# Kernel tuning notes

Hardware: AMD Instinct MI355X
Metric: run time of the kernel (lower is better)

Reference implementation:

```python
import jax, jax.numpy as jnp
import numpy as np

HEADS = 8
DIM_HEAD = 64


def setup_inputs() -> dict:
    key = jax.random.key(0)
    ks = jax.random.split(key, 5)
    B, N, C, coor = 2, 2048, 256, 3
    dim_inner = HEADS * DIM_HEAD  # 512
    # weight scale 1/16 ~ 1/sqrt(256) keeps softmax logits in a sane range
    w_scale = 1.0 / 16.0
    return {
        "x": jax.random.normal(ks[0], (B, N, C, coor), dtype=jnp.float32),
        "Wq": jax.random.normal(ks[1], (dim_inner, C), dtype=jnp.float32) * w_scale,
        "Wk": jax.random.normal(ks[2], (dim_inner, C), dtype=jnp.float32) * w_scale,
        "Wv": jax.random.normal(ks[3], (dim_inner, C), dtype=jnp.float32) * w_scale,
        "Wo": jax.random.normal(ks[4], (C, dim_inner), dtype=jnp.float32) * w_scale,
    }


def _split_heads(t, B, N, coor):
    # b n (h d) c -> b h n (d c)
    t = t.reshape(B, N, HEADS, DIM_HEAD, coor)
    t = t.transpose(0, 2, 1, 3, 4)
    return t.reshape(B, HEADS, N, DIM_HEAD * coor)


def reference(x, Wq, Wk, Wv, Wo):
    B, N, C, coor = x.shape
    # VNLinear: einsum('... i c, o i -> ... o c')
    q = jnp.einsum('bnic,oi->bnoc', x, Wq)
    k = jnp.einsum('bnic,oi->bnoc', x, Wk)
    v = jnp.einsum('bnic,oi->bnoc', x, Wv)
    q = _split_heads(q, B, N, coor)  # (B, H, N, d*c)
    k = _split_heads(k, B, N, coor)
    v = _split_heads(v, B, N, coor)
    scale = (DIM_HEAD * coor) ** -0.5
    sim = jnp.einsum('bhie,bhje->bhij', q, k) * scale  # (B, H, N, N)
    attn = jax.nn.softmax(sim, axis=-1)
    out = jnp.einsum('bhij,bhje->bhie', attn, v)  # (B, H, N, d*c)
    # b h n (d c) -> b n (h d) c
    out = out.reshape(B, HEADS, N, DIM_HEAD, coor).transpose(0, 2, 1, 3, 4)
    out = out.reshape(B, N, HEADS * DIM_HEAD, coor)
    # to_out VNLinear
    return jnp.einsum('bnic,oi->bnoc', out, Wo)  # (B, N, C, 3)
```

## Files before the change

kernel.cpp:

```cpp
#include <hip/hip_runtime.h>

#define HEADS 8
#define DH 64
#define CO 3
#define E 192
#define NSEQ 2048
#define BATCH 2
#define CIN 256
#define DINNER 512
#define NTOK 4096
#define BHTOT 16

typedef __attribute__((ext_vector_type(8))) short bf16x8;
typedef __attribute__((ext_vector_type(4))) short bf16x4;
typedef __attribute__((ext_vector_type(4))) float f32x4;
typedef __attribute__((ext_vector_type(4))) float float4v;

static __device__ inline short f2bf(float f) {
  union { float f; unsigned u; } v; v.f = f;
  unsigned r = (v.u + 0x7FFFu + ((v.u >> 16) & 1u)) >> 16;
  return (short)r;
}

static __device__ inline float bf2f(short s) {
  union { unsigned u; float f; } a;
  a.u = ((unsigned)(unsigned short)s) << 16;
  return a.f;
}

static __device__ inline void load_lds16(const short* g, short* l) {
  __builtin_amdgcn_global_load_lds(
      (const __attribute__((address_space(1))) void*)g,
      (__attribute__((address_space(3))) void*)l, 16, 0, 0);
}


__global__ __launch_bounds__(256) void prep(const float* __restrict__ x,
                                            const float* __restrict__ Wq,
                                            const float* __restrict__ Wk,
                                            const float* __restrict__ Wv,
                                            const float* __restrict__ Wo,
                                            short* __restrict__ xcp,
                                            short* __restrict__ wqkvp,
                                            short* __restrict__ wop) {
  int tid = threadIdx.x;
  if (blockIdx.x < 256) {
    __shared__ short st[12288];
    int mt = blockIdx.x;
    const float* xb = x + (size_t)mt * 12288;
#pragma unroll
    for (int r = 0; r < 12; r++) {
      int idx4 = r * 256 + tid;
      float4v v = *(const float4v*)(xb + idx4 * 4);
#pragma unroll
      for (int e = 0; e < 4; e++) {
        int fp = idx4 * 4 + e;
        int ti = fp / 3, c = fp - ti * 3;
        int tl = ti >> 8, i = ti & 255;
        int ks = i >> 5, qd = (i >> 3) & 3, j = i & 7;
        st[c * 4096 + ks * 512 + (qd * 16 + tl) * 8 + j] = f2bf(v[e]);
      }
    }
    __syncthreads();
    short* dst = xcp;
#pragma unroll
    for (int rep = 0; rep < 6; rep++) {
      int g = rep * 256 + tid;
      int c = g >> 9, rem = g & 511;
      *(bf16x8*)(dst + ((size_t)(c * 256 + mt) * 8) * 512 + rem * 8) =
          *(const bf16x8*)&st[c * 4096 + rem * 8];
    }
    return;
  }
  int idx = (blockIdx.x - 256) * 256 + tid;
  const float qscale = 0.07216878364870323f * 1.4426950408889634f;
  if (idx < 1536 * 256) {
    int o = idx >> 8, i = idx & 255;
    float v;
    if (o < 512) v = Wq[idx] * qscale;
    else if (o < 1024) v = Wk[idx - 512 * 256];
    else v = Wv[idx - 1024 * 256];
    int nt = o >> 4, ln = o & 15, ks = i >> 5, qd = (i >> 3) & 3, j = i & 7;
    wqkvp[((size_t)(nt * 8 + ks)) * 512 + (qd * 16 + ln) * 8 + j] = f2bf(v);
  } else {
    int j0 = idx - 1536 * 256;
    if (j0 < 256 * 512) {
      int o2 = j0 >> 9, i = j0 & 511;
      int nt = o2 >> 4, ln = o2 & 15, ks = i >> 5, qd = (i >> 3) & 3, j = i & 7;
      wop[((size_t)(nt * 16 + ks)) * 512 + (qd * 16 + ln) * 8 + j] = f2bf(Wo[j0]);
    }
  }
}

__global__ __launch_bounds__(256, 4) void qkv_gemm(const short* __restrict__ xcp,
                                                   const short* __restrict__ wqkvp,
                                                   short* __restrict__ qp,
                                                   short* __restrict__ kp,
                                                   short* __restrict__ vp) {
  __shared__ __align__(16) short pool[9216];
  int c = blockIdx.z, ntb = blockIdx.x, mtb = blockIdx.y;
  int tid = threadIdx.x, wave = tid >> 6, lane = tid & 63;
  int ln = lane & 15, quad = lane >> 4;
  int wm = wave >> 1, wn = wave & 1;

  const short* gA = xcp + ((size_t)(c * 256 + mtb * 8) * 8) * 512;

  f32x4 acc[4][2] = {};
#pragma unroll
  for (int i = 0; i < 2; i++) {
    int q = tid + 256 * i, mf = q >> 6, l = q & 63;
    load_lds16(gA + (size_t)(mf * 8) * 512 + l * 8, pool + q * 8);
  }
  for (int ks = 0; ks < 8; ks++) {
    int b = ks & 1;
    __syncthreads();
    if (ks < 7) {
#pragma unroll
      for (int i = 0; i < 2; i++) {
        int q = tid + 256 * i, mf = q >> 6, l = q & 63;
        load_lds16(gA + (size_t)(mf * 8 + ks + 1) * 512 + l * 8,
                   pool + (b ^ 1) * 4096 + q * 8);
      }
    }
    const short* As = pool + b * 4096;
    bf16x8 af[4], bfr[2];
#pragma unroll
    for (int j = 0; j < 2; j++)
      bfr[j] = *(const bf16x8*)(wqkvp +
          (size_t)((ntb * 4 + wn * 2 + j) * 8 + ks) * 512 + lane * 8);
#pragma unroll
    for (int i = 0; i < 4; i++) af[i] = *(const bf16x8*)&As[(wm * 4 + i) * 512 + lane * 8];
#pragma unroll
    for (int i = 0; i < 4; i++)
#pragma unroll
      for (int j = 0; j < 2; j++)
        acc[i][j] = __builtin_amdgcn_mfma_f32_16x16x32_bf16(af[i], bfr[j], acc[i][j], 0, 0, 0);
  }

  int mat = ntb >> 3;
  int h = ntb & 7;
  int b0 = mtb >> 4;
  int bhx = b0 * 8 + h;
  if (mat < 2) {
    __syncthreads();
    short* tp = pool;
#pragma unroll
    for (int i = 0; i < 4; i++)
#pragma unroll
      for (int j = 0; j < 2; j++)
#pragma unroll
        for (int jj = 0; jj < 4; jj++)
          tp[(wm * 64 + i * 16 + quad * 4 + jj) * 72 + wn * 32 + j * 16 + ln] =
              f2bf(acc[i][j][jj]);
    __syncthreads();
    short* dst = (mat == 0) ? qp : kp;
#pragma unroll
    for (int rep = 0; rep < 4; rep++) {
      int gi = rep * 256 + tid;
      int l2 = gi & 15, qd = (gi >> 4) & 3, nf2 = (gi >> 6) & 3,
          esp = (gi >> 8) & 1, kt2 = (gi >> 9) & 1;
      int tl = kt2 * 64 + nf2 * 16 + l2;
      bf16x8 val = *(const bf16x8*)&tp[tl * 72 + esp * 32 + qd * 8];
      int kt = (mtb * 2 + kt2) & 31;
      int es = c * 2 + esp;
      size_t off = (((size_t)((bhx * 32 + kt) * 24) + es * 4 + nf2) * 64 +
                    (size_t)(qd * 16 + l2)) * 8;
      *(bf16x8*)(dst + off) = val;
    }
  } else {
    int q2 = quad ^ (((quad ^ (quad >> 1)) & 1) * 3);
#pragma unroll
    for (int i = 0; i < 4; i++) {
      int kt = (mtb * 2 + wm) & 31;
      int ks2 = (i >> 1) & 1;
      int qd2 = (i * 2 + (q2 >> 1)) & 3;
#pragma unroll
      for (int j = 0; j < 2; j++) {
        int ef = c * 4 + wn * 2 + j;
        size_t off = ((size_t)((bhx * 32 + kt) * 24 + ks2 * 12 + ef)) * 512 +
                     (qd2 * 16 + ln) * 8 + (q2 & 1) * 4;
        bf16x4 val = { f2bf(acc[i][j][0]), f2bf(acc[i][j][1]),
                       f2bf(acc[i][j][2]), f2bf(acc[i][j][3]) };
        *(bf16x4*)(vp + off) = val;
      }
    }
  }
}

__global__ __launch_bounds__(256, 2) void attn(const short* __restrict__ qp,
                                               const short* __restrict__ kp,
                                               const short* __restrict__ vp,
                                               short* __restrict__ opart,
                                               float* __restrict__ lpart) {
  __shared__ __align__(16) short pool[36864];
  int pair = blockIdx.x, qt = blockIdx.y;
  int bh = pair & 15, kh = pair >> 4;
  int tid = threadIdx.x, wave = tid >> 6, lane = tid & 63;
  int ln = lane & 15, quad = lane >> 4;

  bf16x8 qf[2][6];
#pragma unroll
  for (int rg = 0; rg < 2; rg++) {
    int fi = wave * 2 + rg;
    const short* qb = qp +
        ((size_t)(bh * 32 + qt * 2 + (fi >> 2)) * 24 + (fi & 3)) * 512 + lane * 8;
#pragma unroll
    for (int es = 0; es < 6; es++) qf[rg][es] = *(const bf16x8*)(qb + es * 2048);
  }

  float l_r[2] = {0.f, 0.f};
  f32x4 acc[2][12] = {};
  bf16x8 pa[2] = {};
  const short* gKb = kp + (size_t)(bh * 32 + kh * 16) * 12288;
  const short* gVb = vp + (size_t)(bh * 32 + kh * 16) * 12288;

  auto stage_k = [&](int k32) {
    const short* g64 = gKb + (size_t)(k32 >> 1) * 12288;
    int half = k32 & 1;
    short* Kd = pool + (k32 % 3) * 6144;
#pragma unroll
    for (int i = 0; i < 3; i++) {
      int q = i * 256 + tid;
      int f = q >> 6, l = q & 63;
      int es = f >> 1, nfl = f & 1;
      load_lds16(g64 + (size_t)(es * 4 + half * 2 + nfl) * 512 + l * 8, Kd + q * 8);
    }
  };
  auto stage_v = [&](int k32) {
    const short* g64 = gVb + (size_t)(k32 >> 1) * 12288;
    int half = k32 & 1;
    short* Vd = pool + 18432 + (k32 % 3) * 6144;
#pragma unroll
    for (int i = 0; i < 3; i++) {
      int q = i * 256 + tid;
      int f = q >> 6, l = q & 63;
      load_lds16(g64 + (size_t)(half * 12 + f) * 512 + l * 8, Vd + q * 8);
    }
  };

  stage_k(0);
  stage_k(1);
  stage_v(0);
  for (int kt = 0; kt < 32; kt++) {
    asm volatile("s_waitcnt vmcnt(6)" ::: "memory");
    __builtin_amdgcn_s_barrier();
    asm volatile("" ::: "memory");
    if (kt < 30) stage_k(kt + 2);
    if (kt < 31) stage_v(kt + 1);
    const short* Kl = pool + (kt % 3) * 6144;
    const short* Vl = pool + 18432 + ((kt + 2) % 3) * 6144;

    __builtin_amdgcn_s_setprio(1);
    f32x4 s[2][2] = {};
#pragma unroll
    for (int es = 0; es < 6; es++) {
#pragma unroll
      for (int nfl = 0; nfl < 2; nfl++) {
        bf16x8 kf = *(const bf16x8*)&Kl[(es * 2 + nfl) * 512 + lane * 8];
        s[0][nfl] = __builtin_amdgcn_mfma_f32_16x16x32_bf16(kf, qf[0][es], s[0][nfl], 0, 0, 0);
        s[1][nfl] = __builtin_amdgcn_mfma_f32_16x16x32_bf16(kf, qf[1][es], s[1][nfl], 0, 0, 0);
      }
    }
    if (kt > 0) {
#pragma unroll
      for (int ef = 0; ef < 12; ef++) {
        bf16x8 v0 = *(const bf16x8*)&Vl[ef * 512 + lane * 8];
        acc[0][ef] = __builtin_amdgcn_mfma_f32_16x16x32_bf16(pa[0], v0, acc[0][ef], 0, 0, 0);
        acc[1][ef] = __builtin_amdgcn_mfma_f32_16x16x32_bf16(pa[1], v0, acc[1][ef], 0, 0, 0);
      }
    }
    __builtin_amdgcn_s_setprio(0);

#pragma unroll
    for (int rg = 0; rg < 2; rg++) {
      float p0[4], p1[4];
#pragma unroll
      for (int jj = 0; jj < 4; jj++) {
        float e0 = __builtin_amdgcn_exp2f(s[rg][0][jj]);
        float e1 = __builtin_amdgcn_exp2f(s[rg][1][jj]);
        p0[jj] = e0; p1[jj] = e1;
        l_r[rg] += e0;
        l_r[rg] += e1;
      }
      unsigned a0, a1, b0, b1;
      asm("v_cvt_pk_bf16_f32 %0, %1, %2" : "=v"(a0) : "v"(p0[0]), "v"(p0[1]));
      asm("v_cvt_pk_bf16_f32 %0, %1, %2" : "=v"(a1) : "v"(p0[2]), "v"(p0[3]));
      asm("v_cvt_pk_bf16_f32 %0, %1, %2" : "=v"(b0) : "v"(p1[0]), "v"(p1[1]));
      asm("v_cvt_pk_bf16_f32 %0, %1, %2" : "=v"(b1) : "v"(p1[2]), "v"(p1[3]));
      auto r0 = __builtin_amdgcn_permlane32_swap(a0, b0, false, false);
      auto r1 = __builtin_amdgcn_permlane32_swap(a1, b1, false, false);
      union { unsigned u[4]; bf16x8 v; } pk;
      pk.u[0] = r0[0]; pk.u[1] = r1[0]; pk.u[2] = r0[1]; pk.u[3] = r1[1];
      pa[rg] = pk.v;
    }
  }

  __syncthreads();
  {
    const short* Vl = pool + 18432 + 6144;
#pragma unroll
    for (int ef = 0; ef < 12; ef++) {
      bf16x8 v0 = *(const bf16x8*)&Vl[ef * 512 + lane * 8];
      acc[0][ef] = __builtin_amdgcn_mfma_f32_16x16x32_bf16(pa[0], v0, acc[0][ef], 0, 0, 0);
      acc[1][ef] = __builtin_amdgcn_mfma_f32_16x16x32_bf16(pa[1], v0, acc[1][ef], 0, 0, 0);
    }
  }

#pragma unroll
  for (int rg = 0; rg < 2; rg++) {
    l_r[rg] += __shfl_xor(l_r[rg], 16, 64);
    l_r[rg] += __shfl_xor(l_r[rg], 32, 64);
  }

  __syncthreads();
  short* tp = pool;
#pragma unroll
  for (int rg = 0; rg < 2; rg++)
#pragma unroll
    for (int jj = 0; jj < 4; jj++) {
      int row = (wave * 2 + rg) * 16 + quad * 4 + jj;
#pragma unroll
      for (int ef = 0; ef < 12; ef++)
        tp[row * 200 + ef * 16 + ln] = f2bf(acc[rg][ef][jj]);
    }
  __syncthreads();
  const size_t obase = ((size_t)(kh * 16 + bh) * 2048 + qt * 128) * 192;
#pragma unroll
  for (int rep = 0; rep < 12; rep++) {
    int gi = rep * 256 + tid;
    int row = gi / 24, c8 = gi - row * 24;
    *(bf16x8*)(opart + obase + (size_t)row * 192 + c8 * 8) =
        *(const bf16x8*)&tp[row * 200 + c8 * 8];
  }
  int lb = (kh * 16 + bh) * 2048 + qt * 128;
  if (quad == 0) {
#pragma unroll
    for (int rg = 0; rg < 2; rg++)
      lpart[lb + (wave * 2 + rg) * 16 + ln] = l_r[rg];
  }
}

__global__ __launch_bounds__(256) void out_gemm(const short* __restrict__ opart,
                                                const float* __restrict__ lpart,
                                                const short* __restrict__ wop,
                                                float* __restrict__ out) {
  __shared__ __align__(16) float pool_f[12352];
  short* Al = (short*)pool_f;
  int mtb = blockIdx.x;
  int tid = threadIdx.x, wave = tid >> 6, lane = tid & 63;
  int ln = lane & 15, quad = lane >> 4;
  const size_t HSTR = (size_t)16 * 2048 * 192;

#pragma unroll
  for (int rep = 0; rep < 12; rep++) {
    int g = rep * 256 + tid;
    int c = g >> 10, inner = g & 1023;
    int d8 = inner & 7, h = (inner >> 3) & 7, row16 = inner >> 6;
    int t = mtb * 16 + row16, b = t >> 11, n = t & 2047;
    int bh = b * 8 + h;
    size_t src = ((size_t)bh * 2048 + n) * 192 + c * 64 + d8 * 8;
    bf16x8 o1 = *(const bf16x8*)(opart + src);
    bf16x8 o2 = *(const bf16x8*)(opart + HSTR + src);
    float l = lpart[bh * 2048 + n] + lpart[32768 + bh * 2048 + n];
    float inv = 1.f / l;
    bf16x8 r;
#pragma unroll
    for (int j = 0; j < 8; j++) r[j] = f2bf((bf2f(o1[j]) + bf2f(o2[j])) * inv);
    int ks = h * 2 + (d8 >> 2), qd = d8 & 3;
    *(bf16x8*)&Al[c * 8192 + ks * 512 + (qd * 16 + row16) * 8] = r;
  }
  __syncthreads();

  f32x4 acc[3][4] = {};
  for (int ks = 0; ks < 16; ks++) {
    bf16x8 af[3];
#pragma unroll
    for (int c = 0; c < 3; c++) af[c] = *(const bf16x8*)&Al[c * 8192 + ks * 512 + lane * 8];
#pragma unroll
    for (int jf = 0; jf < 4; jf++) {
      int nt = wave * 4 + jf;
      bf16x8 bfr = *(const bf16x8*)(wop + (size_t)(nt * 16 + ks) * 512 + lane * 8);
#pragma unroll
      for (int c = 0; c < 3; c++)
        acc[c][jf] = __builtin_amdgcn_mfma_f32_16x16x32_bf16(af[c], bfr, acc[c][jf], 0, 0, 0);
    }
  }
  __syncthreads();
#pragma unroll
  for (int c = 0; c < 3; c++)
#pragma unroll
    for (int jf = 0; jf < 4; jf++) {
      int o2 = (wave * 4 + jf) * 16 + ln;
#pragma unroll
      for (int jj = 0; jj < 4; jj++)
        pool_f[(quad * 4 + jj) * 772 + o2 * 3 + c] = acc[c][jf][jj];
    }
  __syncthreads();
  float* ob = out + (size_t)mtb * 12288;
#pragma unroll
  for (int rep = 0; rep < 12; rep++) {
    int idx = rep * 256 + tid;
    int row = idx / 192, col4 = idx - row * 192;
    *(float4v*)(ob + row * 768 + col4 * 4) =
        *(const float4v*)(pool_f + row * 772 + col4 * 4);
  }
}

extern "C" void kernel_launch(void* const* d_in, const int* in_sizes, int n_in,
                              void* d_out, int out_size, void* d_ws, size_t ws_size,
                              hipStream_t stream) {
  const float* x  = (const float*)d_in[0];
  const float* Wq = (const float*)d_in[1];
  const float* Wk = (const float*)d_in[2];
  const float* Wv = (const float*)d_in[3];
  const float* Wo = (const float*)d_in[4];
  float* out = (float*)d_out;

  short* ws    = (short*)d_ws;
  short* xcp   = ws;
  short* wqkvp = xcp + 3 * NTOK * CIN;
  short* wop   = wqkvp + 1536 * 256;
  short* qp    = wop + 256 * 512;
  short* kp    = qp + (size_t)BHTOT * NSEQ * E;
  short* vp    = kp + (size_t)BHTOT * NSEQ * E;
  short* opart = vp + (size_t)BHTOT * NSEQ * E;
  float* lpart = (float*)xcp;

  prep<<<2304, 256, 0, stream>>>(x, Wq, Wk, Wv, Wo, xcp, wqkvp, wop);
  qkv_gemm<<<dim3(24, 32, 3), 256, 0, stream>>>(xcp, wqkvp, qp, kp, vp);
  attn<<<dim3(32, 16), 256, 0, stream>>>(qp, kp, vp, opart, lpart);
  out_gemm<<<256, 256, 0, stream>>>(opart, lpart, wop, out);
}
```

Baseline: 155.8 us.

## Load V fragments directly from global into registers, drop LDS V staging

V tiles are now read by each wave straight from global memory into registers instead of being staged through LDS. The PV MFMA now runs in the same iteration as the QK product, replacing the one-iteration-delayed software pipeline. This shrinks LDS use and removes the V LDS reads. In exchange it adds 12 vector registers per lane, and each of the four waves loads the same V data from global/L2 separately. K staging keeps a triple buffer, plus a dummy fourth slot for the tail prefetches.

```diff
diff --git a/kernel.cpp b/kernel.cpp
--- a/kernel.cpp
+++ b/kernel.cpp
@@ -192,7 +192,7 @@
                                                const short* __restrict__ vp,
                                                short* __restrict__ opart,
                                                float* __restrict__ lpart) {
-  __shared__ __align__(16) short pool[36864];
+  __shared__ __align__(16) short pool[25600];
   int pair = blockIdx.x, qt = blockIdx.y;
   int bh = pair & 15, kh = pair >> 4;
   int tid = threadIdx.x, wave = tid >> 6, lane = tid & 63;
@@ -210,14 +210,13 @@
 
   float l_r[2] = {0.f, 0.f};
   f32x4 acc[2][12] = {};
-  bf16x8 pa[2] = {};
   const short* gKb = kp + (size_t)(bh * 32 + kh * 16) * 12288;
   const short* gVb = vp + (size_t)(bh * 32 + kh * 16) * 12288;
 
-  auto stage_k = [&](int k32) {
+  auto stage_k = [&](int k32, int slot) {
     const short* g64 = gKb + (size_t)(k32 >> 1) * 12288;
     int half = k32 & 1;
-    short* Kd = pool + (k32 % 3) * 6144;
+    short* Kd = pool + slot * 6144;
 #pragma unroll
     for (int i = 0; i < 3; i++) {
       int q = i * 256 + tid;
@@ -226,30 +225,24 @@
       load_lds16(g64 + (size_t)(es * 4 + half * 2 + nfl) * 512 + l * 8, Kd + q * 8);
     }
   };
-  auto stage_v = [&](int k32) {
-    const short* g64 = gVb + (size_t)(k32 >> 1) * 12288;
-    int half = k32 & 1;
-    short* Vd = pool + 18432 + (k32 % 3) * 6144;
-#pragma unroll
-    for (int i = 0; i < 3; i++) {
-      int q = i * 256 + tid;
-      int f = q >> 6, l = q & 63;
-      load_lds16(g64 + (size_t)(half * 12 + f) * 512 + l * 8, Vd + q * 8);
-    }
-  };
-
-  stage_k(0);
-  stage_k(1);
-  stage_v(0);
+
+  stage_k(0, 0);
+  stage_k(1, 1);
   for (int kt = 0; kt < 32; kt++) {
-    asm volatile("s_waitcnt vmcnt(6)" ::: "memory");
+    asm volatile("s_waitcnt vmcnt(3)" ::: "memory");
     __builtin_amdgcn_s_barrier();
     asm volatile("" ::: "memory");
-    if (kt < 30) stage_k(kt + 2);
-    if (kt < 31) stage_v(kt + 1);
+
+    const short* gV64 = gVb + (size_t)(kt >> 1) * 12288 + (size_t)(kt & 1) * 6144;
+    bf16x8 vr[12];
+#pragma unroll
+    for (int ef = 0; ef < 12; ef++)
+      vr[ef] = *(const bf16x8*)(gV64 + ef * 512 + lane * 8);
+    asm volatile("" ::: "memory");
+    stage_k((kt + 2) & 31, (kt < 30) ? ((kt + 2) % 3) : 3);
+    asm volatile("" ::: "memory");
+
     const short* Kl = pool + (kt % 3) * 6144;
-    const short* Vl = pool + 18432 + ((kt + 2) % 3) * 6144;
-
     __builtin_amdgcn_s_setprio(1);
     f32x4 s[2][2] = {};
 #pragma unroll
@@ -261,16 +254,9 @@
         s[1][nfl] = __builtin_amdgcn_mfma_f32_16x16x32_bf16(kf, qf[1][es], s[1][nfl], 0, 0, 0);
       }
     }
-    if (kt > 0) {
-#pragma unroll
-      for (int ef = 0; ef < 12; ef++) {
-        bf16x8 v0 = *(const bf16x8*)&Vl[ef * 512 + lane * 8];
-        acc[0][ef] = __builtin_amdgcn_mfma_f32_16x16x32_bf16(pa[0], v0, acc[0][ef], 0, 0, 0);
-        acc[1][ef] = __builtin_amdgcn_mfma_f32_16x16x32_bf16(pa[1], v0, acc[1][ef], 0, 0, 0);
-      }
-    }
     __builtin_amdgcn_s_setprio(0);
 
+    bf16x8 pa[2];
 #pragma unroll
     for (int rg = 0; rg < 2; rg++) {
       float p0[4], p1[4];
@@ -293,17 +279,16 @@
       pk.u[0] = r0[0]; pk.u[1] = r1[0]; pk.u[2] = r0[1]; pk.u[3] = r1[1];
       pa[rg] = pk.v;
     }
-  }
-
-  __syncthreads();
-  {
-    const short* Vl = pool + 18432 + 6144;
+
+    asm volatile("s_waitcnt vmcnt(3)" ::: "memory");
+    __builtin_amdgcn_sched_barrier(0);
+    __builtin_amdgcn_s_setprio(1);
 #pragma unroll
     for (int ef = 0; ef < 12; ef++) {
-      bf16x8 v0 = *(const bf16x8*)&Vl[ef * 512 + lane * 8];
-      acc[0][ef] = __builtin_amdgcn_mfma_f32_16x16x32_bf16(pa[0], v0, acc[0][ef], 0, 0, 0);
-      acc[1][ef] = __builtin_amdgcn_mfma_f32_16x16x32_bf16(pa[1], v0, acc[1][ef], 0, 0, 0);
-    }
+      acc[0][ef] = __builtin_amdgcn_mfma_f32_16x16x32_bf16(pa[0], vr[ef], acc[0][ef], 0, 0, 0);
+      acc[1][ef] = __builtin_amdgcn_mfma_f32_16x16x32_bf16(pa[1], vr[ef], acc[1][ef], 0, 0, 0);
+    }
+    __builtin_amdgcn_s_setprio(0);
   }
 
 #pragma unroll
```

New measurement: 157.5 us. About the same (+1.1%).
